# Optimization experiments

Measured on AMD Instinct MI355X. Metric: run time of the kernel, lower is better.

Reference implementation:

```python
import jax, jax.numpy as jnp
import numpy as np

# Sparse 3D conv (stride-2 downsample) followed by the matching SparseInverseConv3d,
# implemented as rulebook-style gather-GEMM-scatter. Output coordinates of the
# inverse conv are exactly the input coordinates (spconv indice_key semantics).
SPATIAL = (41, 400, 352)          # (D, H, W) voxel grid
K, S, P, DIL = 3, 2, 1, 1          # kernel, stride, padding, dilation
IN_CH, OUT_CH = 32, 64
N_VOX = 120000
BATCH = 2

# static kernel offsets [27, 3]
OFFSETS = np.stack(np.meshgrid(np.arange(K), np.arange(K), np.arange(K), indexing='ij'), -1).reshape(-1, 3)
OUT_SHAPE = tuple((s + 2 * P - DIL * (K - 1) - 1) // S + 1 for s in SPATIAL)  # (21, 200, 176)


def setup_inputs() -> dict:
    key = jax.random.key(0)
    kf, kw1, kw2, kb, kz, ky, kx = jax.random.split(key, 7)
    features = jax.random.normal(kf, (N_VOX, IN_CH), jnp.float32)
    coors = jnp.stack([
        jax.random.randint(kb, (N_VOX,), 0, BATCH),
        jax.random.randint(kz, (N_VOX,), 0, SPATIAL[0]),
        jax.random.randint(ky, (N_VOX,), 0, SPATIAL[1]),
        jax.random.randint(kx, (N_VOX,), 0, SPATIAL[2]),
    ], axis=1).astype(jnp.int32)
    W1 = jax.random.normal(kw1, (K ** 3, IN_CH, OUT_CH), jnp.float32) * (1.0 / np.sqrt(K ** 3 * IN_CH))
    W2 = jax.random.normal(kw2, (K ** 3, OUT_CH, IN_CH), jnp.float32) * (1.0 / np.sqrt(K ** 3 * OUT_CH))
    return {"features": features, "coors": coors, "W1": W1, "W2": W2, "batch_size": BATCH}


def _rulebook(coors, batch_size):
    """Per kernel-offset linear output index + validity. lin == G marks invalid (dump slot)."""
    Dz, Hy, Wx = OUT_SHAPE
    G = batch_size * Dz * Hy * Wx
    b = coors[:, 0]
    c = coors[:, 1:]                                    # [N, 3]
    out_shape = jnp.asarray(OUT_SHAPE, jnp.int32)
    lins, valids = [], []
    for kv in range(K ** 3):
        off = jnp.asarray(OFFSETS[kv], jnp.int32)
        oc = c + P - DIL * off                          # numerator of output coord
        oq = oc // S
        valid = ((oc % S == 0) & (oq >= 0) & (oq < out_shape)).all(-1)
        lin = ((b * Dz + oq[:, 0]) * Hy + oq[:, 1]) * Wx + oq[:, 2]
        lins.append(jnp.where(valid, lin, G))
        valids.append(valid)
    return lins, G


def _spconv_forward(features, coors, W1, W2, batch_size):
    lins, G = _rulebook(coors, batch_size)
    # ---- SparseConv3d: gather(all inputs) -> GEMM per offset -> scatter-add to downsampled grid
    grid = jnp.zeros((G + 1, OUT_CH), features.dtype)   # last row = dump slot
    for kv in range(K ** 3):
        grid = grid.at[lins[kv]].add(features @ W1[kv])
    grid = grid.at[G].set(0.0)                          # clear dump slot -> invalid gathers read 0
    # ---- SparseInverseConv3d: transposed rulebook, output sites = original input coords
    out = jnp.zeros((features.shape[0], IN_CH), features.dtype)
    for kv in range(K ** 3):
        out = out + grid[lins[kv]] @ W2[kv]
    return out


def reference(features, coors, W1, W2, batch_size):
    return _spconv_forward(features, coors, W1, W2, int(batch_size))
```

## Files before the change

kernel.cpp:

```cpp
#include <hip/hip_runtime.h>
#include <stdint.h>


#define N_VOX 120000
#define IC 32
#define OC 64
#define NKV 27
#define DZ 21
#define HY 200
#define WX 176
#define TBL_BITS 20
#define TBL_SIZE (1 << TBL_BITS)
#define TBL_MASK (TBL_SIZE - 1)
#define MAXROWS 480000
#define SPILLCAP 65536

#define OFF_KEYS 0
#define OFF_VALS 4194304
#define OFF_CNT 8388608
#define OFF_ROWS 8388864
#define OFF_FEATB 21348864
#define OFF_W2T 29028864
#define OFF_W1T 29139456
#define OFF_SPILL 29250048
#define OFF_INV 29774336
#define OFF_GRID 81614336
#define WS_NEEDED (OFF_GRID + (size_t)MAXROWS * OC * 2)

typedef __attribute__((ext_vector_type(8))) short short8;
typedef __attribute__((ext_vector_type(4))) float f32x4;

__device__ __forceinline__ uint32_t hash_lin(int lin) {
    return ((uint32_t)lin * 2654435761u) >> (32 - TBL_BITS);
}

__device__ __forceinline__ void atomPkBf16(uint16_t* p, uint32_t v) {
    asm volatile("global_atomic_pk_add_bf16 %0, %1, off" :: "v"(p), "v"(v) : "memory");
}

__device__ __forceinline__ uint32_t pk_bf16(float a, float b) {
    uint32_t x = __float_as_uint(a), y = __float_as_uint(b);
    x = (x + 0x7fffu + ((x >> 16) & 1u)) >> 16;
    y = (y + 0x7fffu + ((y >> 16) & 1u)) >> 16;
    return x | (y << 16);
}
__device__ __forceinline__ uint16_t f2bf(float a) {
    uint32_t x = __float_as_uint(a);
    return (uint16_t)((x + 0x7fffu + ((x >> 16) & 1u)) >> 16);
}
__device__ __forceinline__ float bf2f(uint16_t u) {
    return __uint_as_float(((uint32_t)u) << 16);
}

__global__ void k_init(int* keys, int* counter,
                       const float2* __restrict__ feat2, uint32_t* featb,
                       const float* __restrict__ W1, uint16_t* w1t,
                       const float* __restrict__ W2, uint16_t* w2t) {
    int i = blockIdx.x * blockDim.x + threadIdx.x;
    int stride = gridDim.x * blockDim.x;
    for (int j = i; j < TBL_SIZE; j += stride) keys[j] = -1;
    for (int j = i; j < N_VOX * IC / 2; j += stride) {
        float2 f = feat2[j];
        featb[j] = pk_bf16(f.x, f.y);
    }
    for (int j = i; j < NKV * IC * OC; j += stride) {
        int kv = j >> 11, c = (j >> 6) & 31, o = j & 63;
        w1t[(kv << 11) + (o << 5) + c] = f2bf(W1[j]);
    }
    for (int j = i; j < NKV * OC * IC; j += stride) {
        int kv = j >> 11, o = (j >> 5) & 63, c = j & 31;
        w2t[(kv << 11) + (c << 6) + o] = f2bf(W2[j]);
    }
    if (i == 0) { counter[0] = 0; counter[1] = 0; }
}

__global__ void k_build(const int* __restrict__ coors, int* keys, int* rows) {
    int v = blockIdx.x * blockDim.x + threadIdx.x;
    if (v >= N_VOX) return;
    int b = coors[v * 4 + 0];
    int z = coors[v * 4 + 1];
    int y = coors[v * 4 + 2];
    int x = coors[v * 4 + 3];
#pragma unroll
    for (int kv = 0; kv < NKV; ++kv) {
        int oz = kv / 9, oy = (kv / 3) % 3, ox = kv % 3;
        int az = z + 1 - oz, ay = y + 1 - oy, ax = x + 1 - ox;
        int slot = -1;
        bool valid = (az >= 0) && !(az & 1) && ((az >> 1) < DZ) &&
                     (ay >= 0) && !(ay & 1) && ((ay >> 1) < HY) &&
                     (ax >= 0) && !(ax & 1) && ((ax >> 1) < WX);
        if (valid) {
            int lin = ((b * DZ + (az >> 1)) * HY + (ay >> 1)) * WX + (ax >> 1);
            uint32_t h = hash_lin(lin);
            for (;;) {
                int k = atomicCAS(&keys[h], -1, lin);
                if (k == -1 || k == lin) { slot = (int)h; break; }
                h = (h + 1) & TBL_MASK;
            }
        }
        rows[kv * N_VOX + v] = slot;
    }
}

__global__ __launch_bounds__(256) void k_assign(const int* __restrict__ keys,
                                                int* __restrict__ vals,
                                                int* counter,
                                                int* __restrict__ invt) {
    const int t = threadIdx.x;
    const int s0 = blockIdx.x * 2048 + t * 8;
    const int4 a = ((const int4*)(keys + s0))[0];
    const int4 b = ((const int4*)(keys + s0))[1];
    int k[8] = {a.x, a.y, a.z, a.w, b.x, b.y, b.z, b.w};
    int c = 0;
#pragma unroll
    for (int i = 0; i < 8; ++i) c += (k[i] != -1);

    __shared__ int sc[256];
    __shared__ int base;
    sc[t] = c;
    __syncthreads();
#pragma unroll
    for (int d = 1; d < 256; d <<= 1) {
        int y = (t >= d) ? sc[t - d] : 0;
        __syncthreads();
        sc[t] += y;
        __syncthreads();
    }
    if (t == 255) base = atomicAdd(&counter[0], sc[255]);
    __syncthreads();
    const int total = sc[255];
    int r = base + sc[t] - c;
#pragma unroll
    for (int i = 0; i < 8; ++i) {
        if (k[i] != -1) { vals[s0 + i] = (r < MAXROWS) ? r : -1; ++r; }
    }
    int zs = min(base, MAXROWS), ze = min(base + total, MAXROWS);
    for (int kv = 0; kv < NKV; ++kv)
        for (int i = zs + t; i < ze; i += 256) invt[kv * MAXROWS + i] = -1;
}

__global__ void k_rows_fix(int* rows, const int* __restrict__ vals) {
    int i = blockIdx.x * blockDim.x + threadIdx.x;
    if (i >= NKV * N_VOX) return;
    int s = rows[i];
    rows[i] = (s >= 0) ? vals[s] : -1;
}

__global__ void k_inv(const int* __restrict__ rows, int* invt,
                      int* spill, int* counter) {
    int i = blockIdx.x * blockDim.x + threadIdx.x;
    if (i >= NKV * N_VOX) return;
    int row = rows[i];
    if (row < 0) return;
    int kv = i / N_VOX;
    int v = i - kv * N_VOX;
    int old = atomicCAS(&invt[kv * MAXROWS + row], -1, v);
    if (old != -1) {
        int s = atomicAdd(&counter[1], 1);
        if (s < SPILLCAP) {
            spill[2 * s] = row;
            spill[2 * s + 1] = (kv << 20) | v;
        }
    }
}

__global__ __launch_bounds__(256) void k_scatter_o(
    const uint16_t* __restrict__ featb, const uint16_t* __restrict__ w1t,
    const int* __restrict__ invt, const int* __restrict__ counter,
    uint16_t* __restrict__ gridb) {
    const int wid = threadIdx.x >> 6;
    const int lane = threadIdx.x & 63;
    const int nrows = min(counter[0], MAXROWS);
    const int g0 = (blockIdx.x * 4 + wid) * 16;
    if (g0 >= nrows) return;
    const int lg = lane >> 4;
    const int li = lane & 15;
    const bool rowok = (g0 + li) < nrows;

    f32x4 acc[4] = {{0.f, 0.f, 0.f, 0.f}, {0.f, 0.f, 0.f, 0.f},
                    {0.f, 0.f, 0.f, 0.f}, {0.f, 0.f, 0.f, 0.f}};

#pragma unroll
    for (int kv = 0; kv < NKV; ++kv) {
        const int v = rowok ? invt[(size_t)kv * MAXROWS + g0 + li] : -1;
        if (__ballot(v >= 0) == 0) continue;
        short8 a = {0, 0, 0, 0, 0, 0, 0, 0};
        if (v >= 0) a = *(const short8*)(featb + (size_t)v * IC + lg * 8);
        const uint16_t* w1k = w1t + (kv << 11);
#pragma unroll
        for (int nt = 0; nt < 4; ++nt) {
            const short8 b = *(const short8*)(w1k + (nt * 16 + li) * IC + lg * 8);
            acc[nt] = __builtin_amdgcn_mfma_f32_16x16x32_bf16(a, b, acc[nt], 0, 0, 0);
        }
    }
#pragma unroll
    for (int nt = 0; nt < 4; ++nt) {
#pragma unroll
        for (int rg = 0; rg < 4; ++rg) {
            const int g = g0 + lg * 4 + rg;
            float other = __shfl_xor(acc[nt][rg], 1, 64);
            if ((li & 1) == 0 && g < nrows) {
                *(uint32_t*)(gridb + (size_t)g * OC + nt * 16 + li) =
                    pk_bf16(acc[nt][rg], other);
            }
        }
    }
}

__global__ void k_spill(const uint16_t* __restrict__ featb,
                        const uint16_t* __restrict__ w1t,
                        const int* __restrict__ spill,
                        const int* __restrict__ counter,
                        uint16_t* gridb) {
    const int nspill = min(counter[1], SPILLCAP);
    const int lane = threadIdx.x & 63;
    const int wstride = gridDim.x * (blockDim.x >> 6);
    for (int s = blockIdx.x * (blockDim.x >> 6) + (threadIdx.x >> 6);
         s < nspill; s += wstride) {
        const int row = spill[2 * s];
        const int kvv = spill[2 * s + 1];
        const int kv = kvv >> 20;
        const int v = kvv & 0xFFFFF;
        const uint16_t* f = featb + (size_t)v * IC;
        const uint16_t* wr = w1t + (kv << 11) + lane * IC;
        float acc = 0.f;
#pragma unroll
        for (int c = 0; c < IC; ++c) acc += bf2f(f[c]) * bf2f(wr[c]);
        float other = __shfl_xor(acc, 1, 64);
        if ((lane & 1) == 0)
            atomPkBf16(gridb + (size_t)row * OC + lane, pk_bf16(acc, other));
    }
}

__global__ __launch_bounds__(256) void k_gather_v(
    const uint16_t* __restrict__ gridb, const uint16_t* __restrict__ w2t,
    const int* __restrict__ rows, float* __restrict__ out) {
    const int wid = threadIdx.x >> 6;
    const int lane = threadIdx.x & 63;
    const int v0 = (blockIdx.x * 4 + wid) * 32;
    if (v0 >= N_VOX) return;
    const int lg = lane >> 4;
    const int li = lane & 15;

    f32x4 acc[2][2] = {{{0.f, 0.f, 0.f, 0.f}, {0.f, 0.f, 0.f, 0.f}},
                       {{0.f, 0.f, 0.f, 0.f}, {0.f, 0.f, 0.f, 0.f}}};

    for (int kv = 0; kv < NKV; ++kv) {
        const int* rkv = rows + kv * N_VOX;
        const uint16_t* w2k = w2t + ((size_t)kv << 11);
        short8 b[2][2];
#pragma unroll
        for (int nt = 0; nt < 2; ++nt)
#pragma unroll
            for (int kh = 0; kh < 2; ++kh)
                b[nt][kh] = *(const short8*)(w2k + (nt * 16 + li) * 64 +
                                             kh * 32 + lg * 8);
#pragma unroll
        for (int mt = 0; mt < 2; ++mt) {
            const int v = v0 + mt * 16 + li;
            const int r = rkv[v];
            short8 a0 = {0, 0, 0, 0, 0, 0, 0, 0};
            short8 a1 = {0, 0, 0, 0, 0, 0, 0, 0};
            if (r >= 0) {
                const uint16_t* gr = gridb + (size_t)r * OC;
                a0 = *(const short8*)(gr + lg * 8);
                a1 = *(const short8*)(gr + 32 + lg * 8);
            }
            acc[mt][0] = __builtin_amdgcn_mfma_f32_16x16x32_bf16(a0, b[0][0], acc[mt][0], 0, 0, 0);
            acc[mt][0] = __builtin_amdgcn_mfma_f32_16x16x32_bf16(a1, b[0][1], acc[mt][0], 0, 0, 0);
            acc[mt][1] = __builtin_amdgcn_mfma_f32_16x16x32_bf16(a0, b[1][0], acc[mt][1], 0, 0, 0);
            acc[mt][1] = __builtin_amdgcn_mfma_f32_16x16x32_bf16(a1, b[1][1], acc[mt][1], 0, 0, 0);
        }
    }
#pragma unroll
    for (int mt = 0; mt < 2; ++mt)
#pragma unroll
        for (int nt = 0; nt < 2; ++nt)
#pragma unroll
            for (int rg = 0; rg < 4; ++rg) {
                const int v = v0 + mt * 16 + lg * 4 + rg;
                out[(size_t)v * IC + nt * 16 + li] = acc[mt][nt][rg];
            }
}

extern "C" void kernel_launch(void* const* d_in, const int* in_sizes, int n_in,
                              void* d_out, int out_size, void* d_ws, size_t ws_size,
                              hipStream_t stream) {
    const float* feat = (const float*)d_in[0];
    const int* coors = (const int*)d_in[1];
    const float* W1 = (const float*)d_in[2];
    const float* W2 = (const float*)d_in[3];
    float* out = (float*)d_out;

    if (ws_size < WS_NEEDED) return;

    char* ws = (char*)d_ws;
    int* keys = (int*)(ws + OFF_KEYS);
    int* vals = (int*)(ws + OFF_VALS);
    int* counter = (int*)(ws + OFF_CNT);
    int* rows = (int*)(ws + OFF_ROWS);
    uint32_t* featb = (uint32_t*)(ws + OFF_FEATB);
    uint16_t* w2t = (uint16_t*)(ws + OFF_W2T);
    uint16_t* w1t = (uint16_t*)(ws + OFF_W1T);
    int* spill = (int*)(ws + OFF_SPILL);
    int* invt = (int*)(ws + OFF_INV);
    uint16_t* gridb = (uint16_t*)(ws + OFF_GRID);

    k_init<<<dim3(4096), dim3(256), 0, stream>>>(keys, counter,
                                                 (const float2*)feat, featb,
                                                 W1, w1t, W2, w2t);
    k_build<<<dim3((N_VOX + 255) / 256), dim3(256), 0, stream>>>(coors, keys, rows);
    k_assign<<<dim3(TBL_SIZE / 2048), dim3(256), 0, stream>>>(keys, vals, counter,
                                                              invt);
    k_rows_fix<<<dim3((NKV * N_VOX + 255) / 256), dim3(256), 0, stream>>>(rows, vals);
    k_inv<<<dim3((NKV * N_VOX + 255) / 256), dim3(256), 0, stream>>>(rows, invt,
                                                                     spill, counter);
    k_scatter_o<<<dim3(MAXROWS / 64), dim3(256), 0, stream>>>(
        (const uint16_t*)featb, w1t, invt, counter, gridb);
    k_spill<<<dim3(64), dim3(256), 0, stream>>>((const uint16_t*)featb, w1t,
                                                spill, counter, gridb);
    k_gather_v<<<dim3((N_VOX + 127) / 128), dim3(256), 0, stream>>>(gridb, w2t,
                                                                    rows, out);
}
```

Baseline: 271.0 us.

## Fuse rows_fix with inverse build and software-pipeline gathers in MFMA kernels

```diff
diff --git a/kernel.cpp b/kernel.cpp
--- a/kernel.cpp
+++ b/kernel.cpp
@@ -139,27 +139,23 @@
         for (int i = zs + t; i < ze; i += 256) invt[kv * MAXROWS + i] = -1;
 }
 
-__global__ void k_rows_fix(int* rows, const int* __restrict__ vals) {
+__global__ void k_rows_fix(int* rows, const int* __restrict__ vals,
+                           int* invt, int* spill, int* counter) {
     int i = blockIdx.x * blockDim.x + threadIdx.x;
     if (i >= NKV * N_VOX) return;
     int s = rows[i];
-    rows[i] = (s >= 0) ? vals[s] : -1;
-}
-
-__global__ void k_inv(const int* __restrict__ rows, int* invt,
-                      int* spill, int* counter) {
-    int i = blockIdx.x * blockDim.x + threadIdx.x;
-    if (i >= NKV * N_VOX) return;
-    int row = rows[i];
-    if (row < 0) return;
-    int kv = i / N_VOX;
-    int v = i - kv * N_VOX;
-    int old = atomicCAS(&invt[kv * MAXROWS + row], -1, v);
-    if (old != -1) {
-        int s = atomicAdd(&counter[1], 1);
-        if (s < SPILLCAP) {
-            spill[2 * s] = row;
-            spill[2 * s + 1] = (kv << 20) | v;
+    int row = (s >= 0) ? vals[s] : -1;
+    rows[i] = row;
+    if (row >= 0) {
+        int kv = i / N_VOX;
+        int v = i - kv * N_VOX;
+        int old = atomicCAS(&invt[kv * MAXROWS + row], -1, v);
+        if (old != -1) {
+            int sp = atomicAdd(&counter[1], 1);
+            if (sp < SPILLCAP) {
+                spill[2 * sp] = row;
+                spill[2 * sp + 1] = (kv << 20) | v;
+            }
         }
     }
 }
@@ -176,21 +172,39 @@
     const int lg = lane >> 4;
     const int li = lane & 15;
     const bool rowok = (g0 + li) < nrows;
+    const short8 zz8 = {0, 0, 0, 0, 0, 0, 0, 0};
+
+    int vv[NKV];
+#pragma unroll
+    for (int kv = 0; kv < NKV; ++kv)
+        vv[kv] = rowok ? invt[(size_t)kv * MAXROWS + g0 + li] : -1;
 
     f32x4 acc[4] = {{0.f, 0.f, 0.f, 0.f}, {0.f, 0.f, 0.f, 0.f},
                     {0.f, 0.f, 0.f, 0.f}, {0.f, 0.f, 0.f, 0.f}};
 
+    short8 ap[4];
+#pragma unroll
+    for (int j = 0; j < 3; ++j) {
+        ap[j] = zz8;
+        if (vv[j] >= 0)
+            ap[j] = *(const short8*)(featb + (size_t)vv[j] * IC + lg * 8);
+    }
 #pragma unroll
     for (int kv = 0; kv < NKV; ++kv) {
-        const int v = rowok ? invt[(size_t)kv * MAXROWS + g0 + li] : -1;
-        if (__ballot(v >= 0) == 0) continue;
-        short8 a = {0, 0, 0, 0, 0, 0, 0, 0};
-        if (v >= 0) a = *(const short8*)(featb + (size_t)v * IC + lg * 8);
-        const uint16_t* w1k = w1t + (kv << 11);
-#pragma unroll
-        for (int nt = 0; nt < 4; ++nt) {
-            const short8 b = *(const short8*)(w1k + (nt * 16 + li) * IC + lg * 8);
-            acc[nt] = __builtin_amdgcn_mfma_f32_16x16x32_bf16(a, b, acc[nt], 0, 0, 0);
+        const int kp = kv + 3;
+        if (kp < NKV) {
+            ap[kp & 3] = zz8;
+            if (vv[kp] >= 0)
+                ap[kp & 3] = *(const short8*)(featb + (size_t)vv[kp] * IC + lg * 8);
+        }
+        if (__ballot(vv[kv] >= 0) != 0) {
+            const uint16_t* w1k = w1t + (kv << 11);
+#pragma unroll
+            for (int nt = 0; nt < 4; ++nt) {
+                const short8 b = *(const short8*)(w1k + (nt * 16 + li) * IC + lg * 8);
+                acc[nt] = __builtin_amdgcn_mfma_f32_16x16x32_bf16(ap[kv & 3], b,
+                                                                  acc[nt], 0, 0, 0);
+            }
         }
     }
 #pragma unroll
@@ -237,50 +251,62 @@
     const int* __restrict__ rows, float* __restrict__ out) {
     const int wid = threadIdx.x >> 6;
     const int lane = threadIdx.x & 63;
-    const int v0 = (blockIdx.x * 4 + wid) * 32;
+    const int v0 = (blockIdx.x * 4 + wid) * 16;
     if (v0 >= N_VOX) return;
     const int lg = lane >> 4;
     const int li = lane & 15;
-
-    f32x4 acc[2][2] = {{{0.f, 0.f, 0.f, 0.f}, {0.f, 0.f, 0.f, 0.f}},
-                       {{0.f, 0.f, 0.f, 0.f}, {0.f, 0.f, 0.f, 0.f}}};
-
+    const short8 zz8 = {0, 0, 0, 0, 0, 0, 0, 0};
+
+    int rr[NKV];
+#pragma unroll
+    for (int kv = 0; kv < NKV; ++kv)
+        rr[kv] = rows[kv * N_VOX + v0 + li];
+
+    f32x4 acc[2] = {{0.f, 0.f, 0.f, 0.f}, {0.f, 0.f, 0.f, 0.f}};
+
+    short8 a0p[4], a1p[4];
+#pragma unroll
+    for (int j = 0; j < 3; ++j) {
+        a0p[j] = zz8;
+        a1p[j] = zz8;
+        if (rr[j] >= 0) {
+            const uint16_t* gr = gridb + (size_t)rr[j] * OC;
+            a0p[j] = *(const short8*)(gr + lg * 8);
+            a1p[j] = *(const short8*)(gr + 32 + lg * 8);
+        }
+    }
+#pragma unroll
     for (int kv = 0; kv < NKV; ++kv) {
-        const int* rkv = rows + kv * N_VOX;
-        const uint16_t* w2k = w2t + ((size_t)kv << 11);
-        short8 b[2][2];
-#pragma unroll
-        for (int nt = 0; nt < 2; ++nt)
-#pragma unroll
-            for (int kh = 0; kh < 2; ++kh)
-                b[nt][kh] = *(const short8*)(w2k + (nt * 16 + li) * 64 +
-                                             kh * 32 + lg * 8);
-#pragma unroll
-        for (int mt = 0; mt < 2; ++mt) {
-            const int v = v0 + mt * 16 + li;
-            const int r = rkv[v];
-            short8 a0 = {0, 0, 0, 0, 0, 0, 0, 0};
-            short8 a1 = {0, 0, 0, 0, 0, 0, 0, 0};
-            if (r >= 0) {
-                const uint16_t* gr = gridb + (size_t)r * OC;
-                a0 = *(const short8*)(gr + lg * 8);
-                a1 = *(const short8*)(gr + 32 + lg * 8);
-            }
-            acc[mt][0] = __builtin_amdgcn_mfma_f32_16x16x32_bf16(a0, b[0][0], acc[mt][0], 0, 0, 0);
-            acc[mt][0] = __builtin_amdgcn_mfma_f32_16x16x32_bf16(a1, b[0][1], acc[mt][0], 0, 0, 0);
-            acc[mt][1] = __builtin_amdgcn_mfma_f32_16x16x32_bf16(a0, b[1][0], acc[mt][1], 0, 0, 0);
-            acc[mt][1] = __builtin_amdgcn_mfma_f32_16x16x32_bf16(a1, b[1][1], acc[mt][1], 0, 0, 0);
-        }
-    }
-#pragma unroll
-    for (int mt = 0; mt < 2; ++mt)
-#pragma unroll
-        for (int nt = 0; nt < 2; ++nt)
-#pragma unroll
-            for (int rg = 0; rg < 4; ++rg) {
-                const int v = v0 + mt * 16 + lg * 4 + rg;
-                out[(size_t)v * IC + nt * 16 + li] = acc[mt][nt][rg];
-            }
+        const int kp = kv + 3;
+        if (kp < NKV) {
+            a0p[kp & 3] = zz8;
+            a1p[kp & 3] = zz8;
+            if (rr[kp] >= 0) {
+                const uint16_t* gr = gridb + (size_t)rr[kp] * OC;
+                a0p[kp & 3] = *(const short8*)(gr + lg * 8);
+                a1p[kp & 3] = *(const short8*)(gr + 32 + lg * 8);
+            }
+        }
+        if (__ballot(rr[kv] >= 0) != 0) {
+            const uint16_t* w2k = w2t + ((size_t)kv << 11);
+#pragma unroll
+            for (int nt = 0; nt < 2; ++nt) {
+                const short8 b0 = *(const short8*)(w2k + (nt * 16 + li) * 64 + lg * 8);
+                const short8 b1 = *(const short8*)(w2k + (nt * 16 + li) * 64 + 32 + lg * 8);
+                acc[nt] = __builtin_amdgcn_mfma_f32_16x16x32_bf16(a0p[kv & 3], b0,
+                                                                  acc[nt], 0, 0, 0);
+                acc[nt] = __builtin_amdgcn_mfma_f32_16x16x32_bf16(a1p[kv & 3], b1,
+                                                                  acc[nt], 0, 0, 0);
+            }
+        }
+    }
+#pragma unroll
+    for (int nt = 0; nt < 2; ++nt)
+#pragma unroll
+        for (int rg = 0; rg < 4; ++rg) {
+            const int v = v0 + lg * 4 + rg;
+            out[(size_t)v * IC + nt * 16 + li] = acc[nt][rg];
+        }
 }
 
 extern "C" void kernel_launch(void* const* d_in, const int* in_sizes, int n_in,
@@ -312,13 +338,11 @@
     k_build<<<dim3((N_VOX + 255) / 256), dim3(256), 0, stream>>>(coors, keys, rows);
     k_assign<<<dim3(TBL_SIZE / 2048), dim3(256), 0, stream>>>(keys, vals, counter,
                                                               invt);
-    k_rows_fix<<<dim3((NKV * N_VOX + 255) / 256), dim3(256), 0, stream>>>(rows, vals);
-    k_inv<<<dim3((NKV * N_VOX + 255) / 256), dim3(256), 0, stream>>>(rows, invt,
-                                                                     spill, counter);
+    k_rows_fix<<<dim3((NKV * N_VOX + 255) / 256), dim3(256), 0, stream>>>(
+        rows, vals, invt, spill, counter);
     k_scatter_o<<<dim3(MAXROWS / 64), dim3(256), 0, stream>>>(
         (const uint16_t*)featb, w1t, invt, counter, gridb);
     k_spill<<<dim3(64), dim3(256), 0, stream>>>((const uint16_t*)featb, w1t,
                                                 spill, counter, gridb);
-    k_gather_v<<<dim3((N_VOX + 127) / 128), dim3(256), 0, stream>>>(gridb, w2t,
-                                                                    rows, out);
-}
+    k_gather_v<<<dim3(N_VOX / 64), dim3(256), 0, stream>>>(gridb, w2t, rows, out);
+}
```

After: 299.1 us. 10.4% more time.
